# Optimization experiments

Hardware: AMD Instinct MI355X
Metric: run time of the kernel (lower is better)

The kernel has to match this reference:

```python
import jax, jax.numpy as jnp
import numpy as np


def setup_inputs() -> dict:
    key = jax.random.key(0)
    k1, k2, k3 = jax.random.split(key, 3)
    B, C, H, W = 8, 64, 112, 112
    kh, kw = 5, 5
    return {
        "x": jax.random.normal(k1, (B, C, H, W), dtype=jnp.float32),
        "weight": jax.random.normal(k2, (C, kh, kw), dtype=jnp.float32),
        "bias": jax.random.normal(k3, (C,), dtype=jnp.float32),
        "sign": jnp.ones((1,), dtype=jnp.float32),
        "padding": 2,
        "stride": 1,
        "func_type": 1,
        "alpha": 1,
    }


def _morpho(x, weight, bias, sign, padding, stride, func_type, alpha):
    B, C, H, W = x.shape
    kh, kw = weight.shape[-2:]
    ph = pw = padding
    sh = sw = stride
    H2 = (H + 2 * ph - kh) // sh + 1
    W2 = (W + 2 * pw - kw) // sw + 1
    # sign handling: m*sign*x + (1-m)*x == (m*sign + (1-m)) * x, m detached
    m = jax.lax.stop_gradient((jnp.abs(sign) >= 1e-7).astype(x.dtype))
    s = (m * sign + (1.0 - m)).reshape(-1, 1, 1, 1)  # broadcasts over B or is scalar
    xe = s * x
    xp = jnp.pad(xe, ((0, 0), (0, 0), (ph, ph), (pw, pw)))  # zero pad like F.unfold
    # gather sliding-window taps: [B, C, kh*kw, H2, W2]
    patches = jnp.stack(
        [xp[:, :, i : i + sh * H2 : sh, j : j + sw * W2 : sw]
         for i in range(kh) for j in range(kw)],
        axis=2,
    )
    w = weight.reshape(-1, C, kh * kw, 1, 1)  # (1 or B, C, ks, 1, 1)
    y = patches + w
    if func_type == 0:
        y = y.max(axis=2)
    elif func_type == 1:
        prob = jax.nn.softmax(alpha * y, axis=2)
        y = (y * prob).sum(axis=2)
    elif func_type == 2:
        y = jax.scipy.special.logsumexp(alpha * y, axis=2) / alpha
    else:
        raise NotImplementedError
    if bias is not None:
        y = y + bias.reshape(-1, C, 1, 1)
    y = s * y  # un-apply the sign scaling on the output
    return y  # [B, C, H2, W2]


def reference(x, weight, bias, sign, padding, stride, func_type, alpha):
    return _morpho(x, weight, bias, sign, padding, stride, func_type, alpha)
```

## Files before the change

### kernel.cpp

```cpp
#include <hip/hip_runtime.h>
#include <math.h>

constexpr int B_  = 8;
constexpr int C_  = 64;
constexpr int H_  = 112;
constexpr int W_  = 112;
constexpr int KH  = 5;
constexpr int KW  = 5;
constexpr int PAD = 2;

constexpr int TRR  = 8;
constexpr int LR   = TRR + KH - 1;
constexpr int LCP  = 118;
constexpr int TPB  = 128;
constexpr int NTILES = H_ / TRR;
constexpr int SOUT_LD = 116;
constexpr int NINT = LR * 28;

__global__ __launch_bounds__(TPB, 4)
void morpho_fused(const float* __restrict__ x,
                  const float* __restrict__ weight,
                  const float* __restrict__ bias,
                  const float* __restrict__ sign,
                  const int*   __restrict__ alpha_p,
                  float* __restrict__ out)
{
    __shared__ __align__(16) char smraw[LR * LCP * sizeof(float2)];
    float2 (*sEF)[LCP] = reinterpret_cast<float2 (*)[LCP]>(smraw);

    const int tile  = blockIdx.x;
    const int plane = blockIdx.y;
    const int c     = plane & (C_ - 1);
    const int tid   = threadIdx.x;

    const float sg   = sign[0];
    const float seff = (fabsf(sg) >= 1e-7f) ? sg : 1.0f;
    const float a    = (float)alpha_p[0];
    const float aK   = a * seff;

    const float* xp  = x + (size_t)plane * (H_ * W_);
    const int   row0 = tile * TRR - PAD;

    float4 xv[3];
    int    rr_[3], qq_[3];
    bool   rowok[3], itemok[3];
#pragma unroll
    for (int k = 0; k < 3; ++k) {
        int i  = tid + TPB * k;
        int ic = (i < NINT) ? i : (NINT - 1);
        int r  = ic / 28;
        int q  = ic - r * 28;
        int gr = row0 + r;
        int grc = min(max(gr, 0), H_ - 1);
        xv[k] = *reinterpret_cast<const float4*>(xp + grc * W_ + 4 * q);
        rr_[k] = r; qq_[k] = q;
        rowok[k]  = (gr >= 0) && (gr < H_);
        itemok[k] = (i < NINT);
    }

    const float* wp = weight + c * (KH * KW);
    float su[KH * KW], sv[KH * KW];
#pragma unroll
    for (int k = 0; k < KH * KW; ++k) {
        float wv = wp[k];
        float u  = __expf(a * wv);
        su[k] = u;
        sv[k] = wv * u;
    }

#pragma unroll
    for (int k = 0; k < 3; ++k) {
        if (itemok[k]) {
            float4 v = xv[k];
            bool ok = rowok[k];
            float e0 = ok ? __expf(aK * v.x) : 1.0f;
            float e1 = ok ? __expf(aK * v.y) : 1.0f;
            float e2 = ok ? __expf(aK * v.z) : 1.0f;
            float e3 = ok ? __expf(aK * v.w) : 1.0f;
            float f0 = ok ? (seff * v.x) * e0 : 0.0f;
            float f1 = ok ? (seff * v.y) * e1 : 0.0f;
            float f2 = ok ? (seff * v.z) * e2 : 0.0f;
            float f3 = ok ? (seff * v.w) * e3 : 0.0f;
            float4* dst = reinterpret_cast<float4*>(&sEF[rr_[k]][2 + 4 * qq_[k]]);
            dst[0] = make_float4(e0, f0, e1, f1);
            dst[1] = make_float4(e2, f2, e3, f3);
        }
    }
    if (tid >= 104) {
        int t = tid - 104;
        int r = t >> 1;
        int fi = (t & 1) ? 114 : 0;
        *reinterpret_cast<float4*>(&sEF[r][fi]) = make_float4(1.0f, 0.0f, 1.0f, 0.0f);
    }
    __syncthreads();

    const int ty = tid >> 4;
    const int tx = tid & 15;
    const int c0 = tx * 7;

    float Z[7], Nm[7];
#pragma unroll
    for (int o = 0; o < 7; ++o) { Z[o] = 0.0f; Nm[o] = 0.0f; }

#pragma unroll
    for (int rr = 0; rr < KH; ++rr) {
        float2 ew[11];
#pragma unroll
        for (int jj = 0; jj < 11; ++jj) ew[jj] = sEF[ty + rr][c0 + jj];
#pragma unroll
        for (int j = 0; j < KW; ++j) {
            const float u = su[rr * 5 + j];
            const float v = sv[rr * 5 + j];
#pragma unroll
            for (int o = 0; o < 7; ++o) {
                const float E = ew[o + j].x;
                const float F = ew[o + j].y;
                Z[o]  = fmaf(u, E, Z[o]);
                Nm[o] = fmaf(u, F, fmaf(v, E, Nm[o]));
            }
        }
    }

    __syncthreads();
    float* sOut = reinterpret_cast<float*>(smraw);
    const float sb = seff * bias[c];
#pragma unroll
    for (int o = 0; o < 7; ++o) {
        float val = fmaf(seff * Nm[o], __builtin_amdgcn_rcpf(Z[o]), sb);
        sOut[ty * SOUT_LD + c0 + o] = val;
    }
    __syncthreads();

    float* op = out + (size_t)plane * (H_ * W_) + (size_t)(tile * TRR) * W_;
#pragma unroll
    for (int k = 0; k < 2; ++k) {
        int i = tid + TPB * k;
        if (i < TRR * 28) {
            int r = i / 28;
            int q = i - 28 * r;
            *reinterpret_cast<float4*>(op + r * W_ + 4 * q) =
                *reinterpret_cast<const float4*>(&sOut[r * SOUT_LD + 4 * q]);
        }
    }
}

extern "C" void kernel_launch(void* const* d_in, const int* in_sizes, int n_in,
                              void* d_out, int out_size, void* d_ws, size_t ws_size,
                              hipStream_t stream) {
    const float* x      = (const float*)d_in[0];
    const float* weight = (const float*)d_in[1];
    const float* bias   = (const float*)d_in[2];
    const float* sign   = (const float*)d_in[3];
    const int*   alpha  = (const int*)d_in[7];
    float* out = (float*)d_out;

    dim3 grid(NTILES, B_ * C_);
    morpho_fused<<<grid, TPB, 0, stream>>>(x, weight, bias, sign, alpha, out);
}
```

Measured before the change: 29.42 us.

## Make kernel persistent per plane with double-buffered row tiles and register prefetch

Replaces the 2D grid of short-lived 8-row tile blocks with one 256-thread block per (batch, channel) plane. Each block loops over 16-row tiles, using a double-buffered shared-memory input tile and prefetching the next tile's global rows into registers while it computes the current one. The aim is to amortize the per-block setup (weight exps, bias, sign) and cut the halo overhead per output row. In exchange, the grid shrinks to 512 blocks, so fewer waves are resident per CU to hide latency, and each block runs its tiles one after another.

```diff
diff --git a/kernel.cpp b/kernel.cpp
--- a/kernel.cpp
+++ b/kernel.cpp
@@ -9,27 +9,27 @@
 constexpr int KW  = 5;
 constexpr int PAD = 2;
 
-constexpr int TRR  = 8;
-constexpr int LR   = TRR + KH - 1;
-constexpr int LCP  = 118;
-constexpr int TPB  = 128;
-constexpr int NTILES = H_ / TRR;
+constexpr int TRT = 16;
+constexpr int NT  = H_ / TRT;
+constexpr int LRT = TRT + KH - 1;
+constexpr int LCP = 118;
+constexpr int TPB = 256;
 constexpr int SOUT_LD = 116;
-constexpr int NINT = LR * 28;
+constexpr int NINT = LRT * 28;
+constexpr int NSTORE = TRT * 28;
 
-__global__ __launch_bounds__(TPB, 4)
-void morpho_fused(const float* __restrict__ x,
-                  const float* __restrict__ weight,
-                  const float* __restrict__ bias,
-                  const float* __restrict__ sign,
-                  const int*   __restrict__ alpha_p,
-                  float* __restrict__ out)
+__global__ __launch_bounds__(TPB)
+void morpho_persist(const float* __restrict__ x,
+                    const float* __restrict__ weight,
+                    const float* __restrict__ bias,
+                    const float* __restrict__ sign,
+                    const int*   __restrict__ alpha_p,
+                    float* __restrict__ out)
 {
-    __shared__ __align__(16) char smraw[LR * LCP * sizeof(float2)];
-    float2 (*sEF)[LCP] = reinterpret_cast<float2 (*)[LCP]>(smraw);
+    __shared__ __align__(16) float2 sEF[2][LRT][LCP];
+    __shared__ __align__(16) float  sOut[TRT * SOUT_LD];
 
-    const int tile  = blockIdx.x;
-    const int plane = blockIdx.y;
+    const int plane = blockIdx.x;
     const int c     = plane & (C_ - 1);
     const int tid   = threadIdx.x;
 
@@ -38,24 +38,25 @@
     const float a    = (float)alpha_p[0];
     const float aK   = a * seff;
 
-    const float* xp  = x + (size_t)plane * (H_ * W_);
-    const int   row0 = tile * TRR - PAD;
+    const float* xp = x + (size_t)plane * (H_ * W_);
+    float*       op = out + (size_t)plane * (H_ * W_);
 
-    float4 xv[3];
-    int    rr_[3], qq_[3];
-    bool   rowok[3], itemok[3];
+    int r_[3], q_[3];
+    bool ok_[3];
 #pragma unroll
     for (int k = 0; k < 3; ++k) {
         int i  = tid + TPB * k;
         int ic = (i < NINT) ? i : (NINT - 1);
-        int r  = ic / 28;
-        int q  = ic - r * 28;
-        int gr = row0 + r;
-        int grc = min(max(gr, 0), H_ - 1);
-        xv[k] = *reinterpret_cast<const float4*>(xp + grc * W_ + 4 * q);
-        rr_[k] = r; qq_[k] = q;
-        rowok[k]  = (gr >= 0) && (gr < H_);
-        itemok[k] = (i < NINT);
+        r_[k] = ic / 28;
+        q_[k] = ic - 28 * r_[k];
+        ok_[k] = (i < NINT);
+    }
+
+    float4 xcur[3], xnxt[3];
+#pragma unroll
+    for (int k = 0; k < 3; ++k) {
+        int grc = min(max(-PAD + r_[k], 0), H_ - 1);
+        xcur[k] = *reinterpret_cast<const float4*>(xp + grc * W_ + 4 * q_[k]);
     }
 
     const float* wp = weight + c * (KH * KW);
@@ -67,80 +68,94 @@
         su[k] = u;
         sv[k] = wv * u;
     }
-
-#pragma unroll
-    for (int k = 0; k < 3; ++k) {
-        if (itemok[k]) {
-            float4 v = xv[k];
-            bool ok = rowok[k];
-            float e0 = ok ? __expf(aK * v.x) : 1.0f;
-            float e1 = ok ? __expf(aK * v.y) : 1.0f;
-            float e2 = ok ? __expf(aK * v.z) : 1.0f;
-            float e3 = ok ? __expf(aK * v.w) : 1.0f;
-            float f0 = ok ? (seff * v.x) * e0 : 0.0f;
-            float f1 = ok ? (seff * v.y) * e1 : 0.0f;
-            float f2 = ok ? (seff * v.z) * e2 : 0.0f;
-            float f3 = ok ? (seff * v.w) * e3 : 0.0f;
-            float4* dst = reinterpret_cast<float4*>(&sEF[rr_[k]][2 + 4 * qq_[k]]);
-            dst[0] = make_float4(e0, f0, e1, f1);
-            dst[1] = make_float4(e2, f2, e3, f3);
-        }
-    }
-    if (tid >= 104) {
-        int t = tid - 104;
-        int r = t >> 1;
-        int fi = (t & 1) ? 114 : 0;
-        *reinterpret_cast<float4*>(&sEF[r][fi]) = make_float4(1.0f, 0.0f, 1.0f, 0.0f);
-    }
-    __syncthreads();
+    const float sb = seff * bias[c];
 
     const int ty = tid >> 4;
     const int tx = tid & 15;
     const int c0 = tx * 7;
 
-    float Z[7], Nm[7];
-#pragma unroll
-    for (int o = 0; o < 7; ++o) { Z[o] = 0.0f; Nm[o] = 0.0f; }
+    for (int t = 0; t < NT; ++t) {
+        const int row0 = t * TRT - PAD;
+        float2 (*buf)[LCP] = sEF[t & 1];
 
 #pragma unroll
-    for (int rr = 0; rr < KH; ++rr) {
-        float2 ew[11];
-#pragma unroll
-        for (int jj = 0; jj < 11; ++jj) ew[jj] = sEF[ty + rr][c0 + jj];
-#pragma unroll
-        for (int j = 0; j < KW; ++j) {
-            const float u = su[rr * 5 + j];
-            const float v = sv[rr * 5 + j];
-#pragma unroll
-            for (int o = 0; o < 7; ++o) {
-                const float E = ew[o + j].x;
-                const float F = ew[o + j].y;
-                Z[o]  = fmaf(u, E, Z[o]);
-                Nm[o] = fmaf(u, F, fmaf(v, E, Nm[o]));
+        for (int k = 0; k < 3; ++k) {
+            if (ok_[k]) {
+                int gr = row0 + r_[k];
+                bool ok = (gr >= 0) && (gr < H_);
+                float4 v = xcur[k];
+                float e0 = ok ? __expf(aK * v.x) : 1.0f;
+                float e1 = ok ? __expf(aK * v.y) : 1.0f;
+                float e2 = ok ? __expf(aK * v.z) : 1.0f;
+                float e3 = ok ? __expf(aK * v.w) : 1.0f;
+                float f0 = ok ? (seff * v.x) * e0 : 0.0f;
+                float f1 = ok ? (seff * v.y) * e1 : 0.0f;
+                float f2 = ok ? (seff * v.z) * e2 : 0.0f;
+                float f3 = ok ? (seff * v.w) * e3 : 0.0f;
+                float4* dst = reinterpret_cast<float4*>(&buf[r_[k]][2 + 4 * q_[k]]);
+                dst[0] = make_float4(e0, f0, e1, f1);
+                dst[1] = make_float4(e2, f2, e3, f3);
             }
         }
-    }
+        if (tid < 2 * LRT) {
+            int r  = tid >> 1;
+            int fi = (tid & 1) ? 114 : 0;
+            *reinterpret_cast<float4*>(&buf[r][fi]) = make_float4(1.0f, 0.0f, 1.0f, 0.0f);
+        }
 
-    __syncthreads();
-    float* sOut = reinterpret_cast<float*>(smraw);
-    const float sb = seff * bias[c];
+        if (t + 1 < NT) {
+            const int nrow0 = (t + 1) * TRT - PAD;
 #pragma unroll
-    for (int o = 0; o < 7; ++o) {
-        float val = fmaf(seff * Nm[o], __builtin_amdgcn_rcpf(Z[o]), sb);
-        sOut[ty * SOUT_LD + c0 + o] = val;
-    }
-    __syncthreads();
+            for (int k = 0; k < 3; ++k) {
+                int grc = min(max(nrow0 + r_[k], 0), H_ - 1);
+                xnxt[k] = *reinterpret_cast<const float4*>(xp + grc * W_ + 4 * q_[k]);
+            }
+        }
+        __syncthreads();
 
-    float* op = out + (size_t)plane * (H_ * W_) + (size_t)(tile * TRR) * W_;
+        float Z[7], Nm[7];
 #pragma unroll
-    for (int k = 0; k < 2; ++k) {
-        int i = tid + TPB * k;
-        if (i < TRR * 28) {
-            int r = i / 28;
-            int q = i - 28 * r;
-            *reinterpret_cast<float4*>(op + r * W_ + 4 * q) =
-                *reinterpret_cast<const float4*>(&sOut[r * SOUT_LD + 4 * q]);
+        for (int o = 0; o < 7; ++o) { Z[o] = 0.0f; Nm[o] = 0.0f; }
+
+#pragma unroll
+        for (int rr = 0; rr < KH; ++rr) {
+            float2 ew[11];
+#pragma unroll
+            for (int jj = 0; jj < 11; ++jj) ew[jj] = buf[ty + rr][c0 + jj];
+#pragma unroll
+            for (int j = 0; j < KW; ++j) {
+                const float u = su[rr * 5 + j];
+                const float v = sv[rr * 5 + j];
+#pragma unroll
+                for (int o = 0; o < 7; ++o) {
+                    const float E = ew[o + j].x;
+                    const float F = ew[o + j].y;
+                    Z[o]  = fmaf(u, E, Z[o]);
+                    Nm[o] = fmaf(u, F, fmaf(v, E, Nm[o]));
+                }
+            }
         }
+#pragma unroll
+        for (int o = 0; o < 7; ++o) {
+            sOut[ty * SOUT_LD + c0 + o] =
+                fmaf(seff * Nm[o], __builtin_amdgcn_rcpf(Z[o]), sb);
+        }
+        __syncthreads();
+
+        float* tb = op + (size_t)(t * TRT) * W_;
+#pragma unroll
+        for (int k = 0; k < 2; ++k) {
+            int i = tid + TPB * k;
+            if (i < NSTORE) {
+                int r = i / 28;
+                int q = i - 28 * r;
+                *reinterpret_cast<float4*>(tb + r * W_ + 4 * q) =
+                    *reinterpret_cast<const float4*>(&sOut[r * SOUT_LD + 4 * q]);
+            }
+        }
+
+#pragma unroll
+        for (int k = 0; k < 3; ++k) xcur[k] = xnxt[k];
     }
 }
 
@@ -154,6 +169,6 @@
     const int*   alpha  = (const int*)d_in[7];
     float* out = (float*)d_out;
 
-    dim3 grid(NTILES, B_ * C_);
-    morpho_fused<<<grid, TPB, 0, stream>>>(x, weight, bias, sign, alpha, out);
+    dim3 grid(B_ * C_);
+    morpho_persist<<<grid, TPB, 0, stream>>>(x, weight, bias, sign, alpha, out);
 }
```

Result: no change. 29.82 us (+1.4%).
